# Kernel tuning notes

Measured on AMD Instinct MI355X. Metric: run time of the kernel, lower is better.

## Reference

```python
import jax, jax.numpy as jnp
import numpy as np

N_USERS = 100000
N_ITEMS = 50000
NNZ = 1600000
DIM = 64


def setup_inputs() -> dict:
    key = jax.random.key(0)
    k1, k2, k3, k4, k5, k6, k7 = jax.random.split(key, 7)
    user_x = jax.random.normal(k1, (N_USERS, DIM), dtype=jnp.float32)
    item_x = jax.random.normal(k2, (N_ITEMS, DIM), dtype=jnp.float32)
    # Xavier-uniform-like init for the two weight matrices
    limit = float(np.sqrt(6.0 / (DIM + DIM)))
    user_weight = jax.random.uniform(k3, (DIM, DIM), jnp.float32, -limit, limit)
    item_weight = jax.random.uniform(k4, (DIM, DIM), jnp.float32, -limit, limit)
    # Bipartite adjacency in COO form: ui_graph[r, c] = v ; iu_graph is its transpose
    ui_rows = jax.random.randint(k5, (NNZ,), 0, N_USERS, dtype=jnp.int32)
    ui_cols = jax.random.randint(k6, (NNZ,), 0, N_ITEMS, dtype=jnp.int32)
    ui_vals = jax.random.uniform(k7, (NNZ,), dtype=jnp.float32)
    return {
        "user_x": user_x,
        "item_x": item_x,
        "user_weight": user_weight,
        "item_weight": item_weight,
        "ui_rows": ui_rows,
        "ui_cols": ui_cols,
        "ui_vals": ui_vals,
    }


def _spmm(rows, cols, vals, dense, num_segments):
    # sparse[rows, cols] @ dense  -> gather source rows, scale, scatter-add to dest
    msgs = vals[:, None] * dense[cols]                      # [nnz, d]
    return jax.ops.segment_sum(msgs, rows, num_segments=num_segments)


def reference(user_x, item_x, user_weight, item_weight, ui_rows, ui_cols, ui_vals):
    # dropout p=0.0 -> identity (module default)
    xw_user = user_x @ user_weight                          # [n_users, d]
    xw_item = item_x @ item_weight                          # [n_items, d]
    # out_user = ui_graph @ xw_item ; out_item = iu_graph @ xw_user (iu = ui^T)
    out_user = _spmm(ui_rows, ui_cols, ui_vals, xw_item, N_USERS)
    out_item = _spmm(ui_cols, ui_rows, ui_vals, xw_user, N_ITEMS)
    return jax.nn.relu(out_user), jax.nn.relu(out_item)
```

## Files before the change

kernel.cpp:

```cpp
#include <hip/hip_runtime.h>
#include <hip/hip_bf16.h>

#define N_USERS 100000
#define N_ITEMS 50000
#define NNZ_EDGES 1600000
#define DIM 64

#define BSHIFT_U 8
#define BD_U 256
#define BSHIFT_I 7
#define BD_I 128
#define NBU ((N_USERS + BD_U - 1) / BD_U)
#define NBI ((N_ITEMS + BD_I - 1) / BD_I)
#define NB_MAX 391
#define TILE 4096
#define CAP 4608
#define GEMM_BLKS_U ((N_USERS + 63) / 64)
#define GEMM_BLKS_I ((N_ITEMS + 63) / 64)

__device__ inline unsigned short f32_to_bf16(float f) {
  unsigned u = __float_as_uint(f);
  unsigned r = (u + 0x7FFFu + ((u >> 16) & 1u)) >> 16;
  return (unsigned short)r;
}
__device__ inline float bf16_to_f32(unsigned short h) {
  return __uint_as_float((unsigned)h << 16);
}

__global__ __launch_bounds__(256) void gemm_both_kernel(
    const float* __restrict__ Xu, const float* __restrict__ Wu,
    unsigned short* __restrict__ Yu,
    const float* __restrict__ Xi, const float* __restrict__ Wi,
    unsigned short* __restrict__ Yi,
    int* __restrict__ cur_u, int* __restrict__ cur_i) {
  __shared__ float sXT[64][64];
  __shared__ float sW[64][64];
  const int tid = threadIdx.x;

  if (blockIdx.x == 0) {
    for (int t = tid; t < NBU; t += 256) cur_u[t] = t * CAP;
    for (int t = tid; t < NBI; t += 256) cur_i[t] = t * CAP;
  }

  const float* X; const float* W; unsigned short* Y; int nrows, row_base;
  if (blockIdx.x < GEMM_BLKS_U) {
    X = Xu; W = Wu; Y = Yu; nrows = N_USERS; row_base = blockIdx.x * 64;
  } else {
    X = Xi; W = Wi; Y = Yi; nrows = N_ITEMS; row_base = (blockIdx.x - GEMM_BLKS_U) * 64;
  }

  {
    const float4* Wv = (const float4*)W;
    float4* sWv = (float4*)&sW[0][0];
    #pragma unroll
    for (int i = 0; i < 4; ++i) sWv[tid + i * 256] = Wv[tid + i * 256];
  }
  {
    const int r = tid & 63;
    const int k0 = (tid >> 6) * 16;
    const int grow = row_base + r;
    #pragma unroll
    for (int i = 0; i < 4; ++i) {
      float4 v = make_float4(0.f, 0.f, 0.f, 0.f);
      if (grow < nrows) v = ((const float4*)(X + (size_t)grow * DIM + k0))[i];
      sXT[k0 + i * 4 + 0][r] = v.x;
      sXT[k0 + i * 4 + 1][r] = v.y;
      sXT[k0 + i * 4 + 2][r] = v.z;
      sXT[k0 + i * 4 + 3][r] = v.w;
    }
  }
  __syncthreads();

  const int tx = tid & 15;
  const int ty = tid >> 4;
  float acc[4][4] = {{0.f}};

  #pragma unroll 8
  for (int k = 0; k < 64; ++k) {
    const float4 a = *(const float4*)&sXT[k][ty * 4];
    const float4 b = *(const float4*)&sW[k][tx * 4];
    acc[0][0] = fmaf(a.x, b.x, acc[0][0]);
    acc[0][1] = fmaf(a.x, b.y, acc[0][1]);
    acc[0][2] = fmaf(a.x, b.z, acc[0][2]);
    acc[0][3] = fmaf(a.x, b.w, acc[0][3]);
    acc[1][0] = fmaf(a.y, b.x, acc[1][0]);
    acc[1][1] = fmaf(a.y, b.y, acc[1][1]);
    acc[1][2] = fmaf(a.y, b.z, acc[1][2]);
    acc[1][3] = fmaf(a.y, b.w, acc[1][3]);
    acc[2][0] = fmaf(a.z, b.x, acc[2][0]);
    acc[2][1] = fmaf(a.z, b.y, acc[2][1]);
    acc[2][2] = fmaf(a.z, b.z, acc[2][2]);
    acc[2][3] = fmaf(a.z, b.w, acc[2][3]);
    acc[3][0] = fmaf(a.w, b.x, acc[3][0]);
    acc[3][1] = fmaf(a.w, b.y, acc[3][1]);
    acc[3][2] = fmaf(a.w, b.z, acc[3][2]);
    acc[3][3] = fmaf(a.w, b.w, acc[3][3]);
  }

  #pragma unroll
  for (int r = 0; r < 4; ++r) {
    const int grow = row_base + ty * 4 + r;
    if (grow < nrows) {
      ushort4 o;
      o.x = f32_to_bf16(acc[r][0]);
      o.y = f32_to_bf16(acc[r][1]);
      o.z = f32_to_bf16(acc[r][2]);
      o.w = f32_to_bf16(acc[r][3]);
      *(ushort4*)(Y + (size_t)grow * DIM + tx * 4) = o;
    }
  }
}

__global__ __launch_bounds__(1024) void binning2_kernel(
    const int* __restrict__ rows, const int* __restrict__ cols,
    const float* __restrict__ vals,
    int* __restrict__ cur_u, int* __restrict__ cur_i,
    uint2* __restrict__ out_u, uint2* __restrict__ out_i, int nnz) {
  __shared__ int sh[NB_MAX];
  __shared__ int scnt[NB_MAX];
  __shared__ uint2 sbuf[TILE];
  __shared__ unsigned short sbk[TILE];
  __shared__ int s_w[16];

  const int tid = threadIdx.x, lane = tid & 63, wid = tid >> 6;
  const int tbase = blockIdx.x * TILE;
  const int total = min(TILE, nnz - tbase);

  int er[4], ec[4]; unsigned ev[4];
  #pragma unroll
  for (int k = 0; k < 4; ++k) {
    const int i = tbase + k * 1024 + tid;
    if (i < nnz) {
      er[k] = rows[i];
      ec[k] = cols[i];
      ev[k] = __float_as_uint(vals[i]);
    } else {
      er[k] = -1; ec[k] = 0; ev[k] = 0;
    }
  }

#define BIN_PHASE(BKEXPR, PKEXPR, NB, CUR, OUT)                                \
  {                                                                            \
    for (int j = tid; j < (NB); j += 1024) sh[j] = 0;                          \
    __syncthreads();                                                           \
    int bk[4]; unsigned pk[4];                                                 \
    _Pragma("unroll")                                                          \
    for (int k = 0; k < 4; ++k) {                                              \
      if (er[k] >= 0) {                                                        \
        bk[k] = (BKEXPR); pk[k] = (PKEXPR);                                    \
        atomicAdd(&sh[bk[k]], 1);                                              \
      } else { bk[k] = -1; pk[k] = 0; }                                        \
    }                                                                          \
    __syncthreads();                                                           \
    {                                                                          \
      const int x = (tid < (NB)) ? sh[tid] : 0;                                \
      int incl = x;                                                            \
      _Pragma("unroll")                                                        \
      for (int d = 1; d < 64; d <<= 1) {                                       \
        int t = __shfl_up(incl, d);                                            \
        if (lane >= d) incl += t;                                              \
      }                                                                        \
      if (lane == 63) s_w[wid] = incl;                                         \
      __syncthreads();                                                         \
      if (tid == 0) {                                                          \
        int a = 0;                                                             \
        _Pragma("unroll")                                                      \
        for (int w = 0; w < 16; ++w) { const int t = s_w[w]; s_w[w] = a; a += t; } \
      }                                                                        \
      __syncthreads();                                                         \
      const int excl = s_w[wid] + incl - x;                                    \
      if (tid < (NB)) { scnt[tid] = x; sh[tid] = excl; }                       \
      __syncthreads();                                                         \
    }                                                                          \
    _Pragma("unroll")                                                          \
    for (int k = 0; k < 4; ++k) {                                              \
      if (bk[k] >= 0) {                                                        \
        const int p = atomicAdd(&sh[bk[k]], 1);                                \
        sbuf[p] = make_uint2(pk[k], ev[k]);                                    \
        sbk[p] = (unsigned short)bk[k];                                        \
      }                                                                        \
    }                                                                          \
    __syncthreads();                                                           \
    if (tid < (NB)) {                                                          \
      const int c = scnt[tid];                                                 \
      const int excl = sh[tid] - c;                                            \
      int g = 0;                                                               \
      if (c > 0) g = atomicAdd(&(CUR)[tid], c);                                \
      scnt[tid] = excl;                                                        \
      sh[tid] = g;                                                             \
    }                                                                          \
    __syncthreads();                                                           \
    for (int p = tid; p < total; p += 1024) {                                  \
      const int b = sbk[p];                                                    \
      (OUT)[sh[b] + (p - scnt[b])] = sbuf[p];                                  \
    }                                                                          \
    __syncthreads();                                                           \
  }

  BIN_PHASE(er[k] >> BSHIFT_U,
            ((unsigned)(er[k] & (BD_U - 1)) << 17) | (unsigned)ec[k],
            NBU, cur_u, out_u)
  BIN_PHASE(ec[k] >> BSHIFT_I,
            ((unsigned)(ec[k] & (BD_I - 1)) << 17) | (unsigned)er[k],
            NBI, cur_i, out_i)
#undef BIN_PHASE
}

__global__ __launch_bounds__(1024) void fine_sort_both_kernel(
    uint2* __restrict__ bin_u, const int* __restrict__ cur_u,
    int* __restrict__ uoff, int* __restrict__ uend,
    uint2* __restrict__ bin_i, const int* __restrict__ cur_i,
    int* __restrict__ ioff, int* __restrict__ iend) {
  __shared__ uint2 sbuf[CAP];
  __shared__ int cnt[256];
  __shared__ int s_w[4];
  const int tid = threadIdx.x;
  const int lane = tid & 63, wid = tid >> 6;

  uint2* bin; const int* cur; int* roff; int* rend;
  int b, bd, ndst;
  if (blockIdx.x < NBU) {
    b = blockIdx.x; bd = BD_U; ndst = N_USERS;
    bin = bin_u; cur = cur_u; roff = uoff; rend = uend;
  } else {
    b = blockIdx.x - NBU; bd = BD_I; ndst = N_ITEMS;
    bin = bin_i; cur = cur_i; roff = ioff; rend = iend;
  }
  const int beg = b * CAP;
  const int n = min(cur[b] - beg, CAP);

  if (tid < bd) cnt[tid] = 0;
  __syncthreads();

  for (int i = tid; i < n; i += 1024) {
    const uint2 r = bin[beg + i];
    sbuf[i] = r;
    atomicAdd(&cnt[r.x >> 17], 1);
  }
  __syncthreads();

  int x = 0, incl = 0;
  if (tid < 256) {
    x = (tid < bd) ? cnt[tid] : 0;
    incl = x;
    #pragma unroll
    for (int d = 1; d < 64; d <<= 1) {
      int t = __shfl_up(incl, d);
      if (lane >= d) incl += t;
    }
    if (lane == 63) s_w[wid] = incl;
  }
  __syncthreads();
  if (tid == 0) {
    int a = 0;
    #pragma unroll
    for (int w = 0; w < 4; ++w) { const int t = s_w[w]; s_w[w] = a; a += t; }
  }
  __syncthreads();
  if (tid < 256) {
    const int excl = s_w[wid] + incl - x;
    if (tid < bd) {
      const int base_row = b * bd;
      if (base_row + tid < ndst) {
        roff[base_row + tid] = beg + excl;
        rend[base_row + tid] = beg + excl + x;
      }
      cnt[tid] = excl;
    }
  }
  __syncthreads();

  for (int i = tid; i < n; i += 1024) {
    const uint2 r = sbuf[i];
    const int p = atomicAdd(&cnt[r.x >> 17], 1);
    bin[beg + p] = r;
  }
}

__global__ __launch_bounds__(256) void spmm_both_kernel(
    const uint2* __restrict__ edges_u, const int* __restrict__ uoff,
    const int* __restrict__ uend, const unsigned short* __restrict__ xw_item,
    float* __restrict__ out_user,
    const uint2* __restrict__ edges_i, const int* __restrict__ ioff,
    const int* __restrict__ iend, const unsigned short* __restrict__ xw_user,
    float* __restrict__ out_item) {
  __shared__ uint2 sedge[4][64];
  const int wid = threadIdx.x >> 6, lane = threadIdx.x & 63;
  int d = blockIdx.x * 4 + wid;

  const uint2* edges; const unsigned short* xw; float* out; int beg, end;
  if (d < N_USERS) {
    edges = edges_u; xw = xw_item; out = out_user;
    beg = uoff[d]; end = uend[d];
  } else {
    d -= N_USERS;
    if (d >= N_ITEMS) return;
    edges = edges_i; xw = xw_user; out = out_item;
    beg = ioff[d]; end = iend[d];
  }

  const unsigned short* __restrict__ xwl = xw + lane;
  float acc = 0.f;

  for (int kb = beg; kb < end; kb += 64) {
    const int nbt = min(64, end - kb);
    if (lane < nbt) sedge[wid][lane] = edges[kb + lane];

    int j = 0;
    for (; j + 16 <= nbt; j += 16) {
      uint2 e[16];
      #pragma unroll
      for (int q = 0; q < 16; ++q) e[q] = sedge[wid][j + q];
      unsigned short h[16];
      #pragma unroll
      for (int q = 0; q < 16; ++q)
        h[q] = xwl[(unsigned)((e[q].x & 0x1FFFFu) << 6)];
      #pragma unroll
      for (int q = 0; q < 16; ++q)
        acc = fmaf(__uint_as_float(e[q].y), bf16_to_f32(h[q]), acc);
    }
    for (; j + 8 <= nbt; j += 8) {
      uint2 e[8];
      #pragma unroll
      for (int q = 0; q < 8; ++q) e[q] = sedge[wid][j + q];
      unsigned short h[8];
      #pragma unroll
      for (int q = 0; q < 8; ++q)
        h[q] = xwl[(unsigned)((e[q].x & 0x1FFFFu) << 6)];
      #pragma unroll
      for (int q = 0; q < 8; ++q)
        acc = fmaf(__uint_as_float(e[q].y), bf16_to_f32(h[q]), acc);
    }
    for (; j + 4 <= nbt; j += 4) {
      uint2 e[4];
      #pragma unroll
      for (int q = 0; q < 4; ++q) e[q] = sedge[wid][j + q];
      unsigned short h[4];
      #pragma unroll
      for (int q = 0; q < 4; ++q)
        h[q] = xwl[(unsigned)((e[q].x & 0x1FFFFu) << 6)];
      #pragma unroll
      for (int q = 0; q < 4; ++q)
        acc = fmaf(__uint_as_float(e[q].y), bf16_to_f32(h[q]), acc);
    }
    for (; j < nbt; ++j) {
      const uint2 e = sedge[wid][j];
      acc = fmaf(__uint_as_float(e.y),
                 bf16_to_f32(xwl[(unsigned)((e.x & 0x1FFFFu) << 6)]), acc);
    }
  }
  out[(size_t)d * DIM + lane] = fmaxf(acc, 0.f);
}

extern "C" void kernel_launch(void* const* d_in, const int* in_sizes, int n_in,
                              void* d_out, int out_size, void* d_ws, size_t ws_size,
                              hipStream_t stream) {
  const float* user_x      = (const float*)d_in[0];
  const float* item_x      = (const float*)d_in[1];
  const float* user_weight = (const float*)d_in[2];
  const float* item_weight = (const float*)d_in[3];
  const int*   ui_rows     = (const int*)d_in[4];
  const int*   ui_cols     = (const int*)d_in[5];
  const float* ui_vals     = (const float*)d_in[6];

  float* out_user = (float*)d_out;
  float* out_item = (float*)d_out + (size_t)N_USERS * DIM;

  unsigned short* xw_user = (unsigned short*)d_ws;
  unsigned short* xw_item = xw_user + (size_t)N_USERS * DIM;
  uint2* binA = (uint2*)(xw_item + (size_t)N_ITEMS * DIM);
  uint2* binB = binA + (size_t)NBU * CAP;
  int*   urow_off = (int*)(binB + (size_t)NBI * CAP);
  int*   urow_end = urow_off + N_USERS;
  int*   irow_off = urow_end + N_USERS;
  int*   irow_end = irow_off + N_ITEMS;
  int*   cur_u    = irow_end + N_ITEMS;
  int*   cur_i    = cur_u + NBU;

  gemm_both_kernel<<<GEMM_BLKS_U + GEMM_BLKS_I, 256, 0, stream>>>(
      user_x, user_weight, xw_user, item_x, item_weight, xw_item, cur_u, cur_i);

  const int nblk = (NNZ_EDGES + TILE - 1) / TILE;
  binning2_kernel<<<nblk, 1024, 0, stream>>>(ui_rows, ui_cols, ui_vals,
                                             cur_u, cur_i, binA, binB, NNZ_EDGES);

  fine_sort_both_kernel<<<NBU + NBI, 1024, 0, stream>>>(
      binA, cur_u, urow_off, urow_end,
      binB, cur_i, irow_off, irow_end);

  spmm_both_kernel<<<(N_USERS + N_ITEMS + 3) / 4, 256, 0, stream>>>(
      binA, urow_off, urow_end, xw_item, out_user,
      binB, irow_off, irow_end, xw_user, out_item);
}
```

Before: 137.6 us.

## Split wavefront into half-waves processing two edges with packed bf16x2 gathers

The SpMM kernel now has each lane load a 32-bit pair of bf16 features instead of one 16-bit value, so each half-wave covers a full 64-dim row and the two halves handle alternate edges. The partial sums are combined with a cross-half shuffle, and the output is written as float2. The packed edge key now stores the source index pre-shifted by 6 with the local row in the top 8 bits, removing a shift from the gather address computation. The intent is fewer, wider gather instructions per edge. In exchange it adds a reduction step and an odd-count tail path.

```diff
diff --git a/kernel.cpp b/kernel.cpp
--- a/kernel.cpp
+++ b/kernel.cpp
@@ -18,13 +18,11 @@
 #define GEMM_BLKS_U ((N_USERS + 63) / 64)
 #define GEMM_BLKS_I ((N_ITEMS + 63) / 64)
 
+
 __device__ inline unsigned short f32_to_bf16(float f) {
   unsigned u = __float_as_uint(f);
   unsigned r = (u + 0x7FFFu + ((u >> 16) & 1u)) >> 16;
   return (unsigned short)r;
-}
-__device__ inline float bf16_to_f32(unsigned short h) {
-  return __uint_as_float((unsigned)h << 16);
 }
 
 __global__ __launch_bounds__(256) void gemm_both_kernel(
@@ -198,10 +196,10 @@
   }
 
   BIN_PHASE(er[k] >> BSHIFT_U,
-            ((unsigned)(er[k] & (BD_U - 1)) << 17) | (unsigned)ec[k],
+            ((unsigned)(er[k] & (BD_U - 1)) << 24) | ((unsigned)ec[k] << 6),
             NBU, cur_u, out_u)
   BIN_PHASE(ec[k] >> BSHIFT_I,
-            ((unsigned)(ec[k] & (BD_I - 1)) << 17) | (unsigned)er[k],
+            ((unsigned)(ec[k] & (BD_I - 1)) << 24) | ((unsigned)er[k] << 6),
             NBI, cur_i, out_i)
 #undef BIN_PHASE
 }
@@ -235,7 +233,7 @@
   for (int i = tid; i < n; i += 1024) {
     const uint2 r = bin[beg + i];
     sbuf[i] = r;
-    atomicAdd(&cnt[r.x >> 17], 1);
+    atomicAdd(&cnt[r.x >> 24], 1);
   }
   __syncthreads();
 
@@ -272,7 +270,7 @@
 
   for (int i = tid; i < n; i += 1024) {
     const uint2 r = sbuf[i];
-    const int p = atomicAdd(&cnt[r.x >> 17], 1);
+    const int p = atomicAdd(&cnt[r.x >> 24], 1);
     bin[beg + p] = r;
   }
 }
@@ -286,6 +284,8 @@
     float* __restrict__ out_item) {
   __shared__ uint2 sedge[4][64];
   const int wid = threadIdx.x >> 6, lane = threadIdx.x & 63;
+  const int half = lane >> 5;
+  const int fp = (lane & 31) * 2;
   int d = blockIdx.x * 4 + wid;
 
   const uint2* edges; const unsigned short* xw; float* out; int beg, end;
@@ -299,8 +299,7 @@
     beg = ioff[d]; end = iend[d];
   }
 
-  const unsigned short* __restrict__ xwl = xw + lane;
-  float acc = 0.f;
+  float ax = 0.f, ay = 0.f;
 
   for (int kb = beg; kb < end; kb += 64) {
     const int nbt = min(64, end - kb);
@@ -308,48 +307,44 @@
 
     int j = 0;
     for (; j + 16 <= nbt; j += 16) {
-      uint2 e[16];
-      #pragma unroll
-      for (int q = 0; q < 16; ++q) e[q] = sedge[wid][j + q];
-      unsigned short h[16];
-      #pragma unroll
-      for (int q = 0; q < 16; ++q)
-        h[q] = xwl[(unsigned)((e[q].x & 0x1FFFFu) << 6)];
-      #pragma unroll
-      for (int q = 0; q < 16; ++q)
-        acc = fmaf(__uint_as_float(e[q].y), bf16_to_f32(h[q]), acc);
-    }
-    for (; j + 8 <= nbt; j += 8) {
       uint2 e[8];
       #pragma unroll
-      for (int q = 0; q < 8; ++q) e[q] = sedge[wid][j + q];
-      unsigned short h[8];
+      for (int q = 0; q < 8; ++q) e[q] = sedge[wid][j + 2 * q + half];
+      unsigned g[8];
       #pragma unroll
       for (int q = 0; q < 8; ++q)
-        h[q] = xwl[(unsigned)((e[q].x & 0x1FFFFu) << 6)];
+        g[q] = *(const unsigned*)(xw + ((e[q].x & 0xFFFFC0u) + fp));
       #pragma unroll
-      for (int q = 0; q < 8; ++q)
-        acc = fmaf(__uint_as_float(e[q].y), bf16_to_f32(h[q]), acc);
-    }
-    for (; j + 4 <= nbt; j += 4) {
-      uint2 e[4];
-      #pragma unroll
-      for (int q = 0; q < 4; ++q) e[q] = sedge[wid][j + q];
-      unsigned short h[4];
-      #pragma unroll
-      for (int q = 0; q < 4; ++q)
-        h[q] = xwl[(unsigned)((e[q].x & 0x1FFFFu) << 6)];
-      #pragma unroll
-      for (int q = 0; q < 4; ++q)
-        acc = fmaf(__uint_as_float(e[q].y), bf16_to_f32(h[q]), acc);
-    }
-    for (; j < nbt; ++j) {
+      for (int q = 0; q < 8; ++q) {
+        const float v = __uint_as_float(e[q].y);
+        ax = fmaf(v, __uint_as_float(g[q] << 16), ax);
+        ay = fmaf(v, __uint_as_float(g[q] & 0xFFFF0000u), ay);
+      }
+    }
+    for (; j + 2 <= nbt; j += 2) {
+      const uint2 e = sedge[wid][j + half];
+      const unsigned g = *(const unsigned*)(xw + ((e.x & 0xFFFFC0u) + fp));
+      const float v = __uint_as_float(e.y);
+      ax = fmaf(v, __uint_as_float(g << 16), ax);
+      ay = fmaf(v, __uint_as_float(g & 0xFFFF0000u), ay);
+    }
+    if (j < nbt) {
       const uint2 e = sedge[wid][j];
-      acc = fmaf(__uint_as_float(e.y),
-                 bf16_to_f32(xwl[(unsigned)((e.x & 0x1FFFFu) << 6)]), acc);
-    }
-  }
-  out[(size_t)d * DIM + lane] = fmaxf(acc, 0.f);
+      const unsigned g = *(const unsigned*)(xw + ((e.x & 0xFFFFC0u) + fp));
+      const float v = half ? 0.f : __uint_as_float(e.y);
+      ax = fmaf(v, __uint_as_float(g << 16), ax);
+      ay = fmaf(v, __uint_as_float(g & 0xFFFF0000u), ay);
+    }
+  }
+
+  ax += __shfl_xor(ax, 32);
+  ay += __shfl_xor(ay, 32);
+  if (half == 0) {
+    float2 o;
+    o.x = fmaxf(ax, 0.f);
+    o.y = fmaxf(ay, 0.f);
+    *(float2*)(out + (size_t)d * DIM + fp) = o;
+  }
 }
 
 extern "C" void kernel_launch(void* const* d_in, const int* in_sizes, int n_in,
```

Measured after the change: 146.2 us. 6.2% more time.

## Fuse per-bucket fine sort with SpMM, keeping sorted edges in shared memory

Applied to the files above, without the earlier changes.

Merges the fine-sort and SpMM kernels into one. Each 1024-thread block counting-sorts its bucket's edges into LDS and then has its 16 waves compute the output rows straight from LDS, so the sorted edges are never written back to global memory, no row offset/end arrays are needed, and one launch is dropped. The packed key now stores the column already multiplied by 64 with the local row in the top bits, which removes a shift in the gather. In exchange SpMM parallelism falls to one block per bucket, with waves looping over up to 256 rows, which can unbalance load and lower the number of gathers in flight.

```diff
diff --git a/kernel.cpp b/kernel.cpp
--- a/kernel.cpp
+++ b/kernel.cpp
@@ -17,6 +17,7 @@
 #define CAP 4608
 #define GEMM_BLKS_U ((N_USERS + 63) / 64)
 #define GEMM_BLKS_I ((N_ITEMS + 63) / 64)
+
 
 __device__ inline unsigned short f32_to_bf16(float f) {
   unsigned u = __float_as_uint(f);
@@ -198,33 +199,34 @@
   }
 
   BIN_PHASE(er[k] >> BSHIFT_U,
-            ((unsigned)(er[k] & (BD_U - 1)) << 17) | (unsigned)ec[k],
+            ((unsigned)(er[k] & (BD_U - 1)) << 24) | ((unsigned)ec[k] << 6),
             NBU, cur_u, out_u)
   BIN_PHASE(ec[k] >> BSHIFT_I,
-            ((unsigned)(ec[k] & (BD_I - 1)) << 17) | (unsigned)er[k],
+            ((unsigned)(ec[k] & (BD_I - 1)) << 24) | ((unsigned)er[k] << 6),
             NBI, cur_i, out_i)
 #undef BIN_PHASE
 }
 
-__global__ __launch_bounds__(1024) void fine_sort_both_kernel(
-    uint2* __restrict__ bin_u, const int* __restrict__ cur_u,
-    int* __restrict__ uoff, int* __restrict__ uend,
-    uint2* __restrict__ bin_i, const int* __restrict__ cur_i,
-    int* __restrict__ ioff, int* __restrict__ iend) {
+__global__ __launch_bounds__(1024) void sort_spmm_kernel(
+    const uint2* __restrict__ bin_u, const int* __restrict__ cur_u,
+    const unsigned short* __restrict__ xw_item, float* __restrict__ out_user,
+    const uint2* __restrict__ bin_i, const int* __restrict__ cur_i,
+    const unsigned short* __restrict__ xw_user, float* __restrict__ out_item) {
   __shared__ uint2 sbuf[CAP];
   __shared__ int cnt[256];
+  __shared__ int roff[256];
   __shared__ int s_w[4];
   const int tid = threadIdx.x;
   const int lane = tid & 63, wid = tid >> 6;
 
-  uint2* bin; const int* cur; int* roff; int* rend;
+  const uint2* bin; const int* cur; const unsigned short* xw; float* out;
   int b, bd, ndst;
   if (blockIdx.x < NBU) {
     b = blockIdx.x; bd = BD_U; ndst = N_USERS;
-    bin = bin_u; cur = cur_u; roff = uoff; rend = uend;
+    bin = bin_u; cur = cur_u; xw = xw_item; out = out_user;
   } else {
     b = blockIdx.x - NBU; bd = BD_I; ndst = N_ITEMS;
-    bin = bin_i; cur = cur_i; roff = ioff; rend = iend;
+    bin = bin_i; cur = cur_i; xw = xw_user; out = out_item;
   }
   const int beg = b * CAP;
   const int n = min(cur[b] - beg, CAP);
@@ -232,10 +234,16 @@
   if (tid < bd) cnt[tid] = 0;
   __syncthreads();
 
-  for (int i = tid; i < n; i += 1024) {
-    const uint2 r = bin[beg + i];
-    sbuf[i] = r;
-    atomicAdd(&cnt[r.x >> 17], 1);
+  uint2 rg[5];
+  #pragma unroll
+  for (int k = 0; k < 5; ++k) {
+    const int i = k * 1024 + tid;
+    if (i < n) {
+      rg[k] = bin[beg + i];
+      atomicAdd(&cnt[rg[k].x >> 24], 1);
+    } else {
+      rg[k] = make_uint2(0u, 0u);
+    }
   }
   __syncthreads();
 
@@ -260,96 +268,56 @@
   if (tid < 256) {
     const int excl = s_w[wid] + incl - x;
     if (tid < bd) {
-      const int base_row = b * bd;
-      if (base_row + tid < ndst) {
-        roff[base_row + tid] = beg + excl;
-        rend[base_row + tid] = beg + excl + x;
-      }
+      roff[tid] = excl;
       cnt[tid] = excl;
     }
   }
   __syncthreads();
 
-  for (int i = tid; i < n; i += 1024) {
-    const uint2 r = sbuf[i];
-    const int p = atomicAdd(&cnt[r.x >> 17], 1);
-    bin[beg + p] = r;
-  }
-}
-
-__global__ __launch_bounds__(256) void spmm_both_kernel(
-    const uint2* __restrict__ edges_u, const int* __restrict__ uoff,
-    const int* __restrict__ uend, const unsigned short* __restrict__ xw_item,
-    float* __restrict__ out_user,
-    const uint2* __restrict__ edges_i, const int* __restrict__ ioff,
-    const int* __restrict__ iend, const unsigned short* __restrict__ xw_user,
-    float* __restrict__ out_item) {
-  __shared__ uint2 sedge[4][64];
-  const int wid = threadIdx.x >> 6, lane = threadIdx.x & 63;
-  int d = blockIdx.x * 4 + wid;
-
-  const uint2* edges; const unsigned short* xw; float* out; int beg, end;
-  if (d < N_USERS) {
-    edges = edges_u; xw = xw_item; out = out_user;
-    beg = uoff[d]; end = uend[d];
-  } else {
-    d -= N_USERS;
-    if (d >= N_ITEMS) return;
-    edges = edges_i; xw = xw_user; out = out_item;
-    beg = ioff[d]; end = iend[d];
-  }
+  #pragma unroll
+  for (int k = 0; k < 5; ++k) {
+    const int i = k * 1024 + tid;
+    if (i < n) {
+      const int p = atomicAdd(&cnt[rg[k].x >> 24], 1);
+      sbuf[p] = rg[k];
+    }
+  }
+  __syncthreads();
 
   const unsigned short* __restrict__ xwl = xw + lane;
-  float acc = 0.f;
-
-  for (int kb = beg; kb < end; kb += 64) {
-    const int nbt = min(64, end - kb);
-    if (lane < nbt) sedge[wid][lane] = edges[kb + lane];
-
-    int j = 0;
-    for (; j + 16 <= nbt; j += 16) {
-      uint2 e[16];
-      #pragma unroll
-      for (int q = 0; q < 16; ++q) e[q] = sedge[wid][j + q];
-      unsigned short h[16];
-      #pragma unroll
-      for (int q = 0; q < 16; ++q)
-        h[q] = xwl[(unsigned)((e[q].x & 0x1FFFFu) << 6)];
-      #pragma unroll
-      for (int q = 0; q < 16; ++q)
-        acc = fmaf(__uint_as_float(e[q].y), bf16_to_f32(h[q]), acc);
-    }
-    for (; j + 8 <= nbt; j += 8) {
+  for (int r = wid; r < bd; r += 16) {
+    const int rb = roff[r], re = cnt[r];
+    float acc = 0.f;
+    int j = rb;
+    for (; j + 8 <= re; j += 8) {
       uint2 e[8];
       #pragma unroll
-      for (int q = 0; q < 8; ++q) e[q] = sedge[wid][j + q];
+      for (int q = 0; q < 8; ++q) e[q] = sbuf[j + q];
       unsigned short h[8];
       #pragma unroll
-      for (int q = 0; q < 8; ++q)
-        h[q] = xwl[(unsigned)((e[q].x & 0x1FFFFu) << 6)];
+      for (int q = 0; q < 8; ++q) h[q] = xwl[e[q].x & 0xFFFFC0u];
       #pragma unroll
       for (int q = 0; q < 8; ++q)
         acc = fmaf(__uint_as_float(e[q].y), bf16_to_f32(h[q]), acc);
     }
-    for (; j + 4 <= nbt; j += 4) {
+    for (; j + 4 <= re; j += 4) {
       uint2 e[4];
       #pragma unroll
-      for (int q = 0; q < 4; ++q) e[q] = sedge[wid][j + q];
+      for (int q = 0; q < 4; ++q) e[q] = sbuf[j + q];
       unsigned short h[4];
       #pragma unroll
-      for (int q = 0; q < 4; ++q)
-        h[q] = xwl[(unsigned)((e[q].x & 0x1FFFFu) << 6)];
+      for (int q = 0; q < 4; ++q) h[q] = xwl[e[q].x & 0xFFFFC0u];
       #pragma unroll
       for (int q = 0; q < 4; ++q)
         acc = fmaf(__uint_as_float(e[q].y), bf16_to_f32(h[q]), acc);
     }
-    for (; j < nbt; ++j) {
-      const uint2 e = sedge[wid][j];
-      acc = fmaf(__uint_as_float(e.y),
-                 bf16_to_f32(xwl[(unsigned)((e.x & 0x1FFFFu) << 6)]), acc);
-    }
-  }
-  out[(size_t)d * DIM + lane] = fmaxf(acc, 0.f);
+    for (; j < re; ++j) {
+      const uint2 e = sbuf[j];
+      acc = fmaf(__uint_as_float(e.y), bf16_to_f32(xwl[e.x & 0xFFFFC0u]), acc);
+    }
+    const int grow = b * bd + r;
+    if (grow < ndst) out[(size_t)grow * DIM + lane] = fmaxf(acc, 0.f);
+  }
 }
 
 extern "C" void kernel_launch(void* const* d_in, const int* in_sizes, int n_in,
@@ -370,12 +338,8 @@
   unsigned short* xw_item = xw_user + (size_t)N_USERS * DIM;
   uint2* binA = (uint2*)(xw_item + (size_t)N_ITEMS * DIM);
   uint2* binB = binA + (size_t)NBU * CAP;
-  int*   urow_off = (int*)(binB + (size_t)NBI * CAP);
-  int*   urow_end = urow_off + N_USERS;
-  int*   irow_off = urow_end + N_USERS;
-  int*   irow_end = irow_off + N_ITEMS;
-  int*   cur_u    = irow_end + N_ITEMS;
-  int*   cur_i    = cur_u + NBU;
+  int*   cur_u = (int*)(binB + (size_t)NBI * CAP);
+  int*   cur_i = cur_u + NBU;
 
   gemm_both_kernel<<<GEMM_BLKS_U + GEMM_BLKS_I, 256, 0, stream>>>(
       user_x, user_weight, xw_user, item_x, item_weight, xw_item, cur_u, cur_i);
@@ -384,11 +348,7 @@
   binning2_kernel<<<nblk, 1024, 0, stream>>>(ui_rows, ui_cols, ui_vals,
                                              cur_u, cur_i, binA, binB, NNZ_EDGES);
 
-  fine_sort_both_kernel<<<NBU + NBI, 1024, 0, stream>>>(
-      binA, cur_u, urow_off, urow_end,
-      binB, cur_i, irow_off, irow_end);
-
-  spmm_both_kernel<<<(N_USERS + N_ITEMS + 3) / 4, 256, 0, stream>>>(
-      binA, urow_off, urow_end, xw_item, out_user,
-      binB, irow_off, irow_end, xw_user, out_item);
-}
+  sort_spmm_kernel<<<NBU + NBI, 1024, 0, stream>>>(
+      binA, cur_u, xw_item, out_user,
+      binB, cur_i, xw_user, out_item);
+}
```

Result: faster. 121.4 us (-11.8%).
